# Kernel tuning notes

Hardware: AMD Instinct MI355X
Metric: run time of the kernel (lower is better)

## Reference

```python
import jax, jax.numpy as jnp
import numpy as np

WS = 8          # window size (8x8)
HEADS = 8
DIM_HEAD = 28
SCALE = DIM_HEAD ** -0.5


def _window_partition(t, ws=WS):
    # [b, H, W, c] -> [b, n_windows, ws*ws, c]
    b, H, W, c = t.shape
    t = t.reshape(b, H // ws, ws, W // ws, ws, c)
    t = t.transpose(0, 1, 3, 2, 4, 5)
    return t.reshape(b, (H // ws) * (W // ws), ws * ws, c)


def _window_reverse(t, H, W, ws=WS):
    # [b, n_windows, ws*ws, c] -> [b, H, W, c]
    b = t.shape[0]
    c = t.shape[-1]
    t = t.reshape(b, H // ws, W // ws, ws, ws, c)
    t = t.transpose(0, 1, 3, 2, 4, 5)
    return t.reshape(b, H, W, c)


def _heads_split(t, nh):
    # [b, n, mm, (nh*d)] -> [b, n, nh, mm, d]
    b, n, mm, cd = t.shape
    return t.reshape(b, n, mm, nh, cd // nh).transpose(0, 1, 3, 2, 4)


def setup_inputs() -> dict:
    key = jax.random.key(0)
    ks = jax.random.split(key, 6)
    b, H, W, c = 128, 32, 32, 224
    inner = DIM_HEAD * HEADS  # 224
    return {
        "x": jax.random.normal(ks[0], (b, H, W, c), jnp.float32),
        "Wq": jax.random.normal(ks[1], (c, inner), jnp.float32) * (c ** -0.5),
        "Wkv": jax.random.normal(ks[2], (c, 2 * inner), jnp.float32) * (c ** -0.5),
        "Wout": jax.random.normal(ks[3], (inner, c), jnp.float32) * (inner ** -0.5),
        "bout": jnp.zeros((c,), jnp.float32),
        "pos_emb1": jax.random.normal(ks[4], (1, 1, HEADS // 2, WS * WS, WS * WS), jnp.float32),
        "pos_emb2": jax.random.normal(ks[5], (1, 1, HEADS // 2, 16, 16), jnp.float32),
    }


def reference(x, Wq, Wkv, Wout, bout, pos_emb1, pos_emb2):
    b, H, W, c = x.shape
    nh = HEADS // 2  # heads per branch

    q = x @ Wq                       # [b,H,W,224]
    kv = x @ Wkv
    k, v = jnp.split(kv, 2, axis=-1)

    half = c // 2
    q1, q2 = q[..., :half], q[..., half:]
    k1, k2 = k[..., :half], k[..., half:]
    v1, v2 = v[..., :half], v[..., half:]

    # ----- local branch: attention within each 8x8 window -----
    q1 = _heads_split(_window_partition(q1), nh) * SCALE  # [b,n,nh,64,d]
    k1 = _heads_split(_window_partition(k1), nh)
    v1 = _heads_split(_window_partition(v1), nh)
    sim1 = jnp.einsum('bnhid,bnhjd->bnhij', q1, k1) + pos_emb1
    attn1 = jax.nn.softmax(sim1, axis=-1)
    out1 = jnp.einsum('bnhij,bnhjd->bnhid', attn1, v1)    # [b,n,nh,64,d]
    bN = out1.shape[1]
    out1 = out1.transpose(0, 1, 3, 2, 4).reshape(b, bN, WS * WS, half)

    # ----- global branch: attention across windows (same in-window position) -----
    def part_global(t):
        t = _window_partition(t)                 # [b,n,mm,half]
        t = t.transpose(0, 2, 1, 3)              # [b,mm,n,half]
        return _heads_split(t, nh)               # [b,mm,nh,n,d]
    q2 = part_global(q2) * SCALE
    k2 = part_global(k2)
    v2 = part_global(v2)
    sim2 = jnp.einsum('bnhid,bnhjd->bnhij', q2, k2) + pos_emb2
    attn2 = jax.nn.softmax(sim2, axis=-1)
    out2 = jnp.einsum('bnhij,bnhjd->bnhid', attn2, v2)    # [b,mm,nh,n,d]
    out2 = out2.transpose(0, 1, 3, 2, 4).reshape(b, WS * WS, bN, half)
    out2 = out2.transpose(0, 2, 1, 3)                     # [b,n,mm,half]

    out = jnp.concatenate([out1, out2], axis=-1)          # [b,n,mm,c]
    out = out @ Wout + bout
    return _window_reverse(out, H, W)
```

## Files before the change

### kernel.cpp

```cpp
#include <hip/hip_runtime.h>
#include <stdint.h>

typedef short s8v __attribute__((ext_vector_type(8)));
typedef float f4v __attribute__((ext_vector_type(4)));
typedef unsigned short u16;

#define MFMA16(a, b, c) __builtin_amdgcn_mfma_f32_16x16x32_bf16(a, b, c, 0, 0, 0)
#define SCALE 0.1889822365046136f

__device__ __forceinline__ u16 f2bf(float f) {
  union { float f; uint32_t u; } v;
  v.f = f;
  uint32_t u = v.u;
  u += 0x7fffu + ((u >> 16) & 1u);
  return (u16)(u >> 16);
}

__device__ __forceinline__ void gld_lds16(const void* g, void* l) {
  __builtin_amdgcn_global_load_lds(
      (const __attribute__((address_space(1))) void*)g,
      (__attribute__((address_space(3))) void*)l, 16, 0, 0);
}

__device__ __forceinline__ s8v mk8(ushort4 lo, ushort4 hi) {
  s8v r;
  r[0] = (short)lo.x; r[1] = (short)lo.y; r[2] = (short)lo.z; r[3] = (short)lo.w;
  r[4] = (short)hi.x; r[5] = (short)hi.y; r[6] = (short)hi.z; r[7] = (short)hi.w;
  return r;
}

__global__ void prep_kernel(const float4* __restrict__ x4,
                            const float* __restrict__ Wq,
                            const float* __restrict__ Wkv,
                            const float* __restrict__ Wout,
                            u16* __restrict__ xb,
                            u16* __restrict__ wqkvt,
                            u16* __restrict__ woutt) {
  const int gsz = gridDim.x * blockDim.x;
  const int gt = blockIdx.x * blockDim.x + threadIdx.x;
  for (int i = gt; i < 7340032; i += gsz) {
    float4 v = x4[i];
    ushort4 o;
    o.x = f2bf(v.x); o.y = f2bf(v.y); o.z = f2bf(v.z); o.w = f2bf(v.w);
    ((ushort4*)xb)[i] = o;
  }
  for (int i = gt; i < 768 * 224; i += gsz) {
    const int n = i / 224, k = i - n * 224;
    float v = 0.f;
    if (n < 224) v = Wq[k * 224 + n];
    else if (n < 672) v = Wkv[k * 448 + (n - 224)];
    wqkvt[i] = f2bf(v);
  }
  for (int i = gt; i < 256 * 224; i += gsz) {
    const int n = i / 224, k = i - n * 224;
    const float v = (n < 224) ? Wout[k * 224 + n] : 0.f;
    woutt[i] = f2bf(v);
  }
}

template <int OUT_F32, int NTILES>
__global__ __launch_bounds__(256) void gemm_an(const u16* __restrict__ A,
                                               const u16* __restrict__ Bt,
                                               void* __restrict__ Cp,
                                               const float* __restrict__ bias,
                                               int Nvalid, int ldc) {
  extern __shared__ u16 smem[];
  u16* As  = smem;
  u16* Bs0 = smem + 28672;
  u16* Bs1 = smem + 32768;
  const int tid = threadIdx.x;
  const int wave = tid >> 6, lane = tid & 63;
  const int c16 = lane & 15, g = lane >> 4;
  const int m0 = blockIdx.x * 128;
  const int wm = wave & 1, wn = wave >> 1;

  const int fbw = wave * 1024 + lane * 16;
  for (int rnd = 0; rnd < 14; ++rnd) {
    const int fb = rnd * 4096 + fbw;
    const int row = fb / 448;
    const int off = fb - row * 448;
    gld_lds16(A + (size_t)(m0 + row) * 224 + (off >> 1),
              (char*)As + rnd * 4096 + wave * 1024);
  }

  const int brow0 = fbw >> 6, bcol0 = (fbw & 63) >> 1;

#define STAGE_B(ntile, ktile, bufp)                                           \
  do {                                                                        \
    const int n0s = (ntile) * 128, k0s = (ktile) * 32;                        \
    char* bb = (char*)((bufp) ? Bs1 : Bs0) + wave * 1024;                     \
    gld_lds16(Bt + (size_t)(n0s + brow0) * 224 + k0s + bcol0, bb);            \
    gld_lds16(Bt + (size_t)(n0s + brow0 + 64) * 224 + k0s + bcol0, bb + 4096);\
  } while (0)

  STAGE_B(0, 0, 0);
  __syncthreads();
  int sp = 0;
  for (int nt = 0; nt < NTILES; ++nt) {
    f4v acc[4][4] = {};
    for (int kt = 0; kt < 7; ++kt) {
      const int ns = nt * 7 + kt + 1;
      if (ns < NTILES * 7) {
        const int nnt = ns / 7;
        STAGE_B(nnt, ns - nnt * 7, sp ^ 1);
      }
      const int k0 = kt * 32;
      const u16* Bs = sp ? Bs1 : Bs0;
      s8v af[4], bf[4];
      for (int t = 0; t < 4; ++t)
        af[t] = *(const s8v*)&As[(wm * 64 + t * 16 + c16) * 224 + k0 + g * 8];
      for (int t = 0; t < 4; ++t)
        bf[t] = *(const s8v*)&Bs[(wn * 64 + t * 16 + c16) * 32 + g * 8];
      for (int i = 0; i < 4; ++i)
        for (int j = 0; j < 4; ++j)
          acc[i][j] = MFMA16(af[i], bf[j], acc[i][j]);
      __syncthreads();
      sp ^= 1;
    }
    const int n0 = nt * 128;
    for (int i = 0; i < 4; ++i) {
      const int rowb = m0 + wm * 64 + i * 16 + g * 4;
      for (int j = 0; j < 4; ++j) {
        const int col = n0 + wn * 64 + j * 16 + c16;
        if (col < Nvalid) {
          if (OUT_F32) {
            const float bz = bias[col];
            for (int r = 0; r < 4; ++r)
              ((float*)Cp)[(size_t)(rowb + r) * ldc + col] = acc[i][j][r] + bz;
          } else {
            for (int r = 0; r < 4; ++r)
              ((u16*)Cp)[(size_t)(rowb + r) * ldc + col] = f2bf(acc[i][j][r]);
          }
        }
      }
    }
  }
#undef STAGE_B
}

__global__ __launch_bounds__(256) void attn_local(const u16* __restrict__ qkv,
                                                  const float* __restrict__ pos1,
                                                  u16* __restrict__ attn) {
  extern __shared__ u16 sm[];
  u16* qs = sm;
  u16* ks = sm + 8192;
  u16* vt = sm + 18432;
  u16* pm = sm;
  const int blk = blockIdx.x;
  const int b = blk >> 4, win = blk & 15;
  const int wy = win >> 2, wx = win & 3;
  const int tid = threadIdx.x;
  const int base_s = (b * 32 + wy * 8) * 32 + wx * 8;
  for (int idx = tid; idx < 3584; idx += 256) {
    const int mtx = idx / 1792;
    int rem = idx - mtx * 1792;
    const int h = rem / 448; rem -= h * 448;
    const int t = rem / 7;
    const int c4 = rem - t * 7;
    const int s = base_s + (t >> 3) * 32 + (t & 7);
    const ushort4 v = *(const ushort4*)(qkv + (size_t)s * 672 + mtx * 224 + h * 28 + c4 * 4);
    *(ushort4*)((mtx ? ks : qs) + (h * 64 + t) * 32 + c4 * 4) = v;
  }
  for (int idx = tid; idx < 512; idx += 256) {
    const int mtx = idx >> 8;
    const int h = (idx >> 6) & 3, t = idx & 63;
    const ushort4 z = {0, 0, 0, 0};
    *(ushort4*)((mtx ? ks : qs) + (h * 64 + t) * 32 + 28) = z;
  }
  for (int idx = tid; idx < 1792; idx += 256) {
    const int h = idx / 448;
    int rem = idx - h * 448;
    const int t = rem / 7;
    const int c4 = rem - t * 7;
    const int s = base_s + (t >> 3) * 32 + (t & 7);
    const ushort4 v = *(const ushort4*)(qkv + (size_t)s * 672 + 448 + h * 28 + c4 * 4);
    u16* col = vt + (h * 32 + c4 * 4) * 72 + t;
    col[0] = v.x; col[72] = v.y; col[144] = v.z; col[216] = v.w;
  }
  __syncthreads();
  const int h = tid >> 6, lane = tid & 63;
  const int c16 = lane & 15, g = lane >> 4;
  s8v af[4], bf[4];
  for (int t = 0; t < 4; ++t) af[t] = *(const s8v*)&qs[(h * 64 + t * 16 + c16) * 32 + g * 8];
  for (int t = 0; t < 4; ++t) bf[t] = *(const s8v*)&ks[(h * 64 + t * 16 + c16) * 32 + g * 8];
  const f4v fz = {0.f, 0.f, 0.f, 0.f};
  f4v sc[4][4];
  for (int i = 0; i < 4; ++i)
    for (int j = 0; j < 4; ++j)
      sc[i][j] = MFMA16(af[i], bf[j], fz);
  float lrow[4][4];
  const float* ph = pos1 + h * 4096;
  for (int i = 0; i < 4; ++i) {
    for (int r = 0; r < 4; ++r) {
      const int irow = i * 16 + g * 4 + r;
      float mx = -1e30f;
      for (int j = 0; j < 4; ++j) {
        const float v = sc[i][j][r] * SCALE + ph[irow * 64 + j * 16 + c16];
        sc[i][j][r] = v;
        mx = fmaxf(mx, v);
      }
      for (int d = 1; d < 16; d <<= 1) mx = fmaxf(mx, __shfl_xor(mx, d, 64));
      float sum = 0.f;
      for (int j = 0; j < 4; ++j) {
        const float e = __expf(sc[i][j][r] - mx);
        sc[i][j][r] = e;
        sum += e;
      }
      for (int d = 1; d < 16; d <<= 1) sum += __shfl_xor(sum, d, 64);
      lrow[i][r] = sum;
    }
  }
  __syncthreads();
  for (int i = 0; i < 4; ++i)
    for (int r = 0; r < 4; ++r) {
      const int irow = i * 16 + g * 4 + r;
      for (int j = 0; j < 4; ++j)
        pm[(h * 64 + irow) * 72 + j * 16 + c16] = f2bf(sc[i][j][r]);
    }
  f4v o[4][2] = {};
  for (int kk = 0; kk < 2; ++kk) {
    s8v ap[4], bv[2];
    for (int t = 0; t < 4; ++t)
      ap[t] = *(const s8v*)&pm[(h * 64 + t * 16 + c16) * 72 + kk * 32 + g * 8];
    for (int t = 0; t < 2; ++t)
      bv[t] = *(const s8v*)&vt[(h * 32 + t * 16 + c16) * 72 + kk * 32 + g * 8];
    for (int i = 0; i < 4; ++i)
      for (int j = 0; j < 2; ++j)
        o[i][j] = MFMA16(ap[i], bv[j], o[i][j]);
  }
  for (int i = 0; i < 4; ++i)
    for (int r = 0; r < 4; ++r) {
      const int irow = i * 16 + g * 4 + r;
      const int s = base_s + (irow >> 3) * 32 + (irow & 7);
      const float inv = 1.f / lrow[i][r];
      for (int j = 0; j < 2; ++j) {
        const int d = j * 16 + c16;
        if (d < 28)
          attn[(size_t)s * 224 + h * 28 + d] = f2bf(o[i][j][r] * inv);
      }
    }
}

__global__ __launch_bounds__(256) void attn_global(const u16* __restrict__ qkv,
                                                   const float* __restrict__ pos2,
                                                   u16* __restrict__ attn) {
  __shared__ u16 p2[4][16][32];
  const int blk = blockIdx.x;
  const int b = blk >> 4, ig = blk & 15;
  const int tid = threadIdx.x;
  const int w = tid >> 6, lane = tid & 63;
  const int c16 = lane & 15, g = lane >> 4;
  const int i = ig * 4 + w;
  const int y = i >> 3, x = i & 7;
  const int sc16 = (b * 32 + (c16 >> 2) * 8 + y) * 32 + (c16 & 3) * 8 + x;
  const u16* rowp = qkv + (size_t)sc16 * 672;
  const f4v fz = {0.f, 0.f, 0.f, 0.f};
  const ushort4 z4 = {0, 0, 0, 0};
  for (int h = 0; h < 4; ++h) {
    const int qo = 112 + h * 28, ko = 336 + h * 28, vo = 560 + h * 28;
    const ushort4 qlo = *(const ushort4*)(rowp + qo + g * 8);
    const ushort4 qhi = (g < 3) ? *(const ushort4*)(rowp + qo + g * 8 + 4) : z4;
    const ushort4 klo = *(const ushort4*)(rowp + ko + g * 8);
    const ushort4 khi = (g < 3) ? *(const ushort4*)(rowp + ko + g * 8 + 4) : z4;
    const s8v aq = mk8(qlo, qhi);
    const s8v bk = mk8(klo, khi);
    const f4v s = MFMA16(aq, bk, fz);
    const float* ph = pos2 + h * 256;
    float l[4];
    for (int r = 0; r < 4; ++r) {
      const float v = s[r] * SCALE + ph[(g * 4 + r) * 16 + c16];
      float mx = v;
      for (int d = 1; d < 16; d <<= 1) mx = fmaxf(mx, __shfl_xor(mx, d, 64));
      const float e = __expf(v - mx);
      float sum = e;
      for (int d = 1; d < 16; d <<= 1) sum += __shfl_xor(sum, d, 64);
      l[r] = sum;
      p2[w][g * 4 + r][c16] = f2bf(e);
      p2[w][g * 4 + r][c16 + 16] = 0;
    }
    const s8v ap = *(const s8v*)&p2[w][c16][g * 8];
    f4v o[2];
    for (int nt = 0; nt < 2; ++nt) {
      s8v bv = {0, 0, 0, 0, 0, 0, 0, 0};
      if (g < 2) {
        const int d = nt * 16 + c16;
        if (d < 28) {
          for (int e = 0; e < 8; ++e) {
            const int j = g * 8 + e;
            const int sj = (b * 32 + (j >> 2) * 8 + y) * 32 + (j & 3) * 8 + x;
            bv[e] = (short)qkv[(size_t)sj * 672 + vo + d];
          }
        }
      }
      o[nt] = MFMA16(ap, bv, fz);
    }
    for (int nt = 0; nt < 2; ++nt)
      for (int r = 0; r < 4; ++r) {
        const int d = nt * 16 + c16;
        if (d < 28) {
          const int wi = g * 4 + r;
          const int sw = (b * 32 + (wi >> 2) * 8 + y) * 32 + (wi & 3) * 8 + x;
          attn[(size_t)sw * 224 + 112 + h * 28 + d] = f2bf(o[nt][r] / l[r]);
        }
      }
  }
}

extern "C" void kernel_launch(void* const* d_in, const int* in_sizes, int n_in,
                              void* d_out, int out_size, void* d_ws, size_t ws_size,
                              hipStream_t stream) {
  const float* x    = (const float*)d_in[0];
  const float* Wq   = (const float*)d_in[1];
  const float* Wkv  = (const float*)d_in[2];
  const float* Wout = (const float*)d_in[3];
  const float* bout = (const float*)d_in[4];
  const float* pos1 = (const float*)d_in[5];
  const float* pos2 = (const float*)d_in[6];
  char* ws = (char*)d_ws;
  u16* qkv   = (u16*)ws;
  u16* xb    = (u16*)(ws + 176160768);
  u16* attn  = xb;
  u16* wqkvt = (u16*)(ws + 234881024);
  u16* woutt = (u16*)(ws + 235225088);

  prep_kernel<<<dim3(1024), 256, 0, stream>>>(
      (const float4*)x, Wq, Wkv, Wout, xb, wqkvt, woutt);

  gemm_an<0, 6><<<dim3(1024), 256, 73728, stream>>>(xb, wqkvt, qkv, nullptr, 672, 672);

  attn_local<<<dim3(2048), 256, 55296, stream>>>(qkv, pos1, attn);
  attn_global<<<dim3(2048), 256, 0, stream>>>(qkv, pos2, attn);

  gemm_an<1, 2><<<dim3(1024), 256, 73728, stream>>>(attn, woutt, d_out, bout, 224, 224);
}
```

Before: 427.8 us.

## Pad LDS strides in GEMM, halve M tile, stage global-attention QKV in LDS

Result: slower. 446.7 us (+4.4%).

```diff
diff --git a/kernel.cpp b/kernel.cpp
--- a/kernel.cpp
+++ b/kernel.cpp
@@ -20,13 +20,6 @@
   __builtin_amdgcn_global_load_lds(
       (const __attribute__((address_space(1))) void*)g,
       (__attribute__((address_space(3))) void*)l, 16, 0, 0);
-}
-
-__device__ __forceinline__ s8v mk8(ushort4 lo, ushort4 hi) {
-  s8v r;
-  r[0] = (short)lo.x; r[1] = (short)lo.y; r[2] = (short)lo.z; r[3] = (short)lo.w;
-  r[4] = (short)hi.x; r[5] = (short)hi.y; r[6] = (short)hi.z; r[7] = (short)hi.w;
-  return r;
 }
 
 __global__ void prep_kernel(const float4* __restrict__ x4,
@@ -66,38 +59,45 @@
                                                int Nvalid, int ldc) {
   extern __shared__ u16 smem[];
   u16* As  = smem;
-  u16* Bs0 = smem + 28672;
-  u16* Bs1 = smem + 32768;
+  u16* Bs0 = smem + 14848;
+  u16* Bs1 = smem + 19968;
   const int tid = threadIdx.x;
   const int wave = tid >> 6, lane = tid & 63;
   const int c16 = lane & 15, g = lane >> 4;
-  const int m0 = blockIdx.x * 128;
+  const int m0 = blockIdx.x * 64;
   const int wm = wave & 1, wn = wave >> 1;
 
-  const int fbw = wave * 1024 + lane * 16;
-  for (int rnd = 0; rnd < 14; ++rnd) {
-    const int fb = rnd * 4096 + fbw;
-    const int row = fb / 448;
-    const int off = fb - row * 448;
-    gld_lds16(A + (size_t)(m0 + row) * 224 + (off >> 1),
-              (char*)As + rnd * 4096 + wave * 1024);
-  }
-
-  const int brow0 = fbw >> 6, bcol0 = (fbw & 63) >> 1;
+  for (int rnd = 0; rnd < 8; ++rnd) {
+    const int chunk = rnd * 256 + tid;
+    if (chunk < 1856) {
+      const int row = chunk / 29;
+      const int off = chunk - row * 29;
+      const int srcoff = (off < 28) ? off * 8 : 0;
+      gld_lds16(A + (size_t)(m0 + row) * 224 + srcoff, (char*)As + chunk * 16);
+    }
+  }
 
 #define STAGE_B(ntile, ktile, bufp)                                           \
   do {                                                                        \
     const int n0s = (ntile) * 128, k0s = (ktile) * 32;                        \
-    char* bb = (char*)((bufp) ? Bs1 : Bs0) + wave * 1024;                     \
-    gld_lds16(Bt + (size_t)(n0s + brow0) * 224 + k0s + bcol0, bb);            \
-    gld_lds16(Bt + (size_t)(n0s + brow0 + 64) * 224 + k0s + bcol0, bb + 4096);\
+    char* bb = (char*)((bufp) ? Bs1 : Bs0);                                   \
+    for (int rr = 0; rr < 3; ++rr) {                                          \
+      const int chunk = rr * 256 + tid;                                       \
+      if (chunk < 640) {                             \
+        const int row = chunk / 5;                                            \
+        const int off = chunk - row * 5;                                      \
+        const int srcoff = (off < 4) ? off * 8 : 0;                           \
+        gld_lds16(Bt + (size_t)(n0s + row) * 224 + k0s + srcoff,              \
+                  bb + chunk * 16);                                           \
+      }                                                                       \
+    }                                                                         \
   } while (0)
 
   STAGE_B(0, 0, 0);
   __syncthreads();
   int sp = 0;
   for (int nt = 0; nt < NTILES; ++nt) {
-    f4v acc[4][4] = {};
+    f4v acc[2][4] = {};
     for (int kt = 0; kt < 7; ++kt) {
       const int ns = nt * 7 + kt + 1;
       if (ns < NTILES * 7) {
@@ -106,20 +106,20 @@
       }
       const int k0 = kt * 32;
       const u16* Bs = sp ? Bs1 : Bs0;
-      s8v af[4], bf[4];
+      s8v af[2], bf[4];
+      for (int t = 0; t < 2; ++t)
+        af[t] = *(const s8v*)&As[(wm * 32 + t * 16 + c16) * 232 + k0 + g * 8];
       for (int t = 0; t < 4; ++t)
-        af[t] = *(const s8v*)&As[(wm * 64 + t * 16 + c16) * 224 + k0 + g * 8];
-      for (int t = 0; t < 4; ++t)
-        bf[t] = *(const s8v*)&Bs[(wn * 64 + t * 16 + c16) * 32 + g * 8];
-      for (int i = 0; i < 4; ++i)
+        bf[t] = *(const s8v*)&Bs[(wn * 64 + t * 16 + c16) * 40 + g * 8];
+      for (int i = 0; i < 2; ++i)
         for (int j = 0; j < 4; ++j)
           acc[i][j] = MFMA16(af[i], bf[j], acc[i][j]);
       __syncthreads();
       sp ^= 1;
     }
     const int n0 = nt * 128;
-    for (int i = 0; i < 4; ++i) {
-      const int rowb = m0 + wm * 64 + i * 16 + g * 4;
+    for (int i = 0; i < 2; ++i) {
+      const int rowb = m0 + wm * 32 + i * 16 + g * 4;
       for (int j = 0; j < 4; ++j) {
         const int col = n0 + wn * 64 + j * 16 + c16;
         if (col < Nvalid) {
@@ -244,26 +244,52 @@
 __global__ __launch_bounds__(256) void attn_global(const u16* __restrict__ qkv,
                                                    const float* __restrict__ pos2,
                                                    u16* __restrict__ attn) {
-  __shared__ u16 p2[4][16][32];
+  extern __shared__ u16 smg[];
+  u16* qs = smg;
+  u16* ks = smg + 8192;
+  u16* vt = smg + 16384;
+  u16* p2 = smg + 24576;
   const int blk = blockIdx.x;
   const int b = blk >> 4, ig = blk & 15;
   const int tid = threadIdx.x;
+  for (int idx = tid; idx < 5376; idx += 256) {
+    const int seg = idx / 1792;
+    int rem = idx - seg * 1792;
+    const int row = rem / 28;
+    const int c4 = rem - row * 28;
+    const int w = row >> 4, j = row & 15;
+    const int ii = ig * 4 + w;
+    const int y = ii >> 3, x = ii & 7;
+    const int s = (b * 32 + (j >> 2) * 8 + y) * 32 + (j & 3) * 8 + x;
+    const int hq = c4 / 7, d4 = c4 - hq * 7;
+    const ushort4 v = *(const ushort4*)(qkv + (size_t)s * 672 + 112 + seg * 224 + c4 * 4);
+    if (seg < 2) {
+      *(ushort4*)((seg ? ks : qs) + ((w * 4 + hq) * 16 + j) * 32 + d4 * 4) = v;
+    } else {
+      u16* col = vt + ((w * 4 + hq) * 32 + d4 * 4) * 16 + j;
+      col[0] = v.x; col[16] = v.y; col[32] = v.z; col[48] = v.w;
+    }
+  }
+  for (int idx = tid; idx < 512; idx += 256) {
+    const ushort4 z = {0, 0, 0, 0};
+    *(ushort4*)(((idx & 256) ? ks : qs) + (idx & 255) * 32 + 28) = z;
+  }
+  {
+    const ushort4 z = {0, 0, 0, 0};
+    const int w = tid >> 6, hq = (tid >> 4) & 3;
+    const int dd = 28 + ((tid >> 2) & 3), j4 = tid & 3;
+    *(ushort4*)(vt + ((w * 4 + hq) * 32 + dd) * 16 + j4 * 4) = z;
+  }
+  __syncthreads();
   const int w = tid >> 6, lane = tid & 63;
   const int c16 = lane & 15, g = lane >> 4;
   const int i = ig * 4 + w;
   const int y = i >> 3, x = i & 7;
-  const int sc16 = (b * 32 + (c16 >> 2) * 8 + y) * 32 + (c16 & 3) * 8 + x;
-  const u16* rowp = qkv + (size_t)sc16 * 672;
+  const int w4 = w * 4;
   const f4v fz = {0.f, 0.f, 0.f, 0.f};
-  const ushort4 z4 = {0, 0, 0, 0};
   for (int h = 0; h < 4; ++h) {
-    const int qo = 112 + h * 28, ko = 336 + h * 28, vo = 560 + h * 28;
-    const ushort4 qlo = *(const ushort4*)(rowp + qo + g * 8);
-    const ushort4 qhi = (g < 3) ? *(const ushort4*)(rowp + qo + g * 8 + 4) : z4;
-    const ushort4 klo = *(const ushort4*)(rowp + ko + g * 8);
-    const ushort4 khi = (g < 3) ? *(const ushort4*)(rowp + ko + g * 8 + 4) : z4;
-    const s8v aq = mk8(qlo, qhi);
-    const s8v bk = mk8(klo, khi);
+    const s8v aq = *(const s8v*)&qs[((w4 + h) * 16 + c16) * 32 + g * 8];
+    const s8v bk = *(const s8v*)&ks[((w4 + h) * 16 + c16) * 32 + g * 8];
     const f4v s = MFMA16(aq, bk, fz);
     const float* ph = pos2 + h * 256;
     float l[4];
@@ -275,23 +301,15 @@
       float sum = e;
       for (int d = 1; d < 16; d <<= 1) sum += __shfl_xor(sum, d, 64);
       l[r] = sum;
-      p2[w][g * 4 + r][c16] = f2bf(e);
-      p2[w][g * 4 + r][c16 + 16] = 0;
-    }
-    const s8v ap = *(const s8v*)&p2[w][c16][g * 8];
+      p2[(w * 16 + g * 4 + r) * 32 + c16] = f2bf(e);
+      p2[(w * 16 + g * 4 + r) * 32 + c16 + 16] = 0;
+    }
+    const s8v ap = *(const s8v*)&p2[(w * 16 + c16) * 32 + g * 8];
     f4v o[2];
     for (int nt = 0; nt < 2; ++nt) {
       s8v bv = {0, 0, 0, 0, 0, 0, 0, 0};
-      if (g < 2) {
-        const int d = nt * 16 + c16;
-        if (d < 28) {
-          for (int e = 0; e < 8; ++e) {
-            const int j = g * 8 + e;
-            const int sj = (b * 32 + (j >> 2) * 8 + y) * 32 + (j & 3) * 8 + x;
-            bv[e] = (short)qkv[(size_t)sj * 672 + vo + d];
-          }
-        }
-      }
+      if (g < 2)
+        bv = *(const s8v*)&vt[((w4 + h) * 32 + nt * 16 + c16) * 16 + g * 8];
       o[nt] = MFMA16(ap, bv, fz);
     }
     for (int nt = 0; nt < 2; ++nt)
@@ -326,10 +344,10 @@
   prep_kernel<<<dim3(1024), 256, 0, stream>>>(
       (const float4*)x, Wq, Wkv, Wout, xb, wqkvt, woutt);
 
-  gemm_an<0, 6><<<dim3(1024), 256, 73728, stream>>>(xb, wqkvt, qkv, nullptr, 672, 672);
+  gemm_an<0, 6><<<dim3(2048), 256, 50176, stream>>>(xb, wqkvt, qkv, nullptr, 672, 672);
 
   attn_local<<<dim3(2048), 256, 55296, stream>>>(qkv, pos1, attn);
-  attn_global<<<dim3(2048), 256, 0, stream>>>(qkv, pos2, attn);
-
-  gemm_an<1, 2><<<dim3(1024), 256, 73728, stream>>>(attn, woutt, d_out, bout, 224, 224);
-}
+  attn_global<<<dim3(2048), 256, 53248, stream>>>(qkv, pos2, attn);
+
+  gemm_an<1, 2><<<dim3(2048), 256, 50176, stream>>>(attn, woutt, d_out, bout, 224, 224);
+}
```
